# Kernel optimization log

Hardware: AMD Instinct MI355X
Metric: run time of the kernel (lower is better)

The kernel has to match this reference:

```python
import jax, jax.numpy as jnp
import numpy as np

POOL = (2, 2, 2)   # LPPool3d kernel == stride
KH, KW = 3, 3      # unfold kernel
EPS = 1e-6


def setup_inputs() -> dict:
    key = jax.random.key(0)
    k1, k2, k3 = jax.random.split(key, 3)
    x = jax.random.normal(k1, (32, 8, 4, 256, 256), dtype=jnp.float32)
    patch_dim = 8 * (4 // POOL[0]) * KH * KW  # 144
    out_dim = 128
    lin_w = jax.random.normal(k2, (out_dim, patch_dim), dtype=jnp.float32) * (1.0 / np.sqrt(patch_dim))
    lin_b = jax.random.normal(k3, (out_dim,), dtype=jnp.float32) * 0.01
    return {"x": x, "lin_w": lin_w, "lin_b": lin_b}


def reference(x, lin_w, lin_b):
    N, C, D, H, W = x.shape
    kd, kh, kw = POOL
    # LPPool3d with p=2, stride==kernel: (sum of squares in window)^(1/2)
    xr = (x * x).reshape(N, C, D // kd, kd, H // kh, kh, W // kw, kw)
    pooled = jnp.sqrt(xr.sum(axis=(3, 5, 7)))  # (N, C, Dp, Hp, Wp)
    Dp, Hp, Wp = pooled.shape[2], pooled.shape[3], pooled.shape[4]
    # merge depth into channels: permute(0,2,1,3,4).view(N, Dp*C, Hp, Wp)
    merged = pooled.transpose(0, 2, 1, 3, 4).reshape(N, Dp * C, Hp, Wp)
    MC = Dp * C
    Ho, Wo = Hp - KH + 1, Wp - KW + 1
    # im2col matching torch.nn.Unfold ordering: (channel, kh, kw) flattened
    slices = [merged[:, :, i:i + Ho, j:j + Wo] for i in range(KH) for j in range(KW)]
    patches = jnp.stack(slices, axis=2)                 # (N, MC, KH*KW, Ho, Wo)
    patches = patches.reshape(N, MC * KH * KW, Ho * Wo) # (N, patch_dim, L)
    patches = patches.transpose(0, 2, 1)                # (N, L, patch_dim)
    # per-patch linear + CELU (alpha=1)
    proj = jnp.einsum('nlk,ok->nlo', patches, lin_w) + lin_b  # (N, L, out_dim)
    act = jax.nn.celu(proj)
    # aggregate over patches, then L2-normalize with clamped norm
    agg = act.mean(axis=1)                              # (N, out_dim)
    norm = jnp.maximum(jnp.linalg.norm(agg, axis=1, keepdims=True), EPS)
    return agg / norm
```

## Files before the change

kernel.cpp:

```cpp
#include <hip/hip_runtime.h>
#include <math.h>

#define NB   32
#define C    8
#define D    4
#define H    256
#define W    256
#define HP   128
#define WP   128
#define MC   16
#define HO   126
#define WO   126
#define PATCH 144
#define OUTD 128
#define NL   (HO*WO)
#define HOG  6
#define NGRP (HO/HOG)
#define PROWS 9
#define BROW 168
#define NPOOLB 2048

typedef float  f32x4  __attribute__((ext_vector_type(4)));
typedef __bf16 bf16x8 __attribute__((ext_vector_type(8)));

__global__ __launch_bounds__(256, 4)
void pool_kernel(const float* __restrict__ x, __bf16* __restrict__ Pg) {
    int t = threadIdx.x;
    int wp2 = t & 63;
    int dph = (t >> 6) & 1;
    int g = blockIdx.x*2 + (t >> 7);
    int hp = g & 127, n = g >> 7;

    const float* xn = x + (size_t)n * (C*D*H*W) + (size_t)(2*dph) * (H*W)
                        + (2*hp)*W + 4*wp2;
    bf16x8 pk0, pk1;
#pragma unroll 2
    for (int c = 0; c < 8; c++) {
        const float* xb = xn + (size_t)c * (D*H*W);
        f32x4 a0 = *(const f32x4*)(xb);
        f32x4 a1 = *(const f32x4*)(xb + W);
        f32x4 a2 = *(const f32x4*)(xb + H*W);
        f32x4 a3 = *(const f32x4*)(xb + H*W + W);
        float s0 = a0.x*a0.x + a0.y*a0.y + a1.x*a1.x + a1.y*a1.y
                 + a2.x*a2.x + a2.y*a2.y + a3.x*a3.x + a3.y*a3.y;
        float s1 = a0.z*a0.z + a0.w*a0.w + a1.z*a1.z + a1.w*a1.w
                 + a2.z*a2.z + a2.w*a2.w + a3.z*a3.z + a3.w*a3.w;
        pk0[c] = (__bf16)sqrtf(s0);
        pk1[c] = (__bf16)sqrtf(s1);
    }
    __bf16* pr = Pg + ((size_t)n*HP + hp) * (WP*MC);
    *(bf16x8*)&pr[(2*wp2    )*16 + dph*8] = pk0;
    *(bf16x8*)&pr[(2*wp2 + 1)*16 + dph*8] = pk1;
}

__global__ __launch_bounds__(256, 2)
void gemm_kernel(const __bf16* __restrict__ Pg, const float* __restrict__ lin_w,
                 const float* __restrict__ lin_b, float* __restrict__ accg) {
    __shared__ __align__(16) char smem[PROWS*128*32 + OUTD*BROW*2];
    __bf16* Pl   = (__bf16*)smem;
    __bf16* Blds = (__bf16*)(smem + PROWS*128*32);

    int blk = blockIdx.x;
    int g = blk % NGRP, n = blk / NGRP;
    int ho0 = g * HOG;
    int t = threadIdx.x;
    int wave = t >> 6, lane = t & 63, quad = lane >> 4, l16 = lane & 15;

    {
        const f32x4* src = (const f32x4*)(Pg + ((size_t)n*HP + ho0) * (WP*MC));
        f32x4* dst = (f32x4*)Pl;
#pragma unroll
        for (int r = 0; r < 8; r++) dst[r*256 + t] = src[r*256 + t];
        f32x4 z = {};
        dst[8*256 + t] = z;
    }
    {
        int o = t & 127, kh = t >> 7;
#pragma unroll 4
        for (int kk = 0; kk < 80; kk++) {
            int kn = kh*80 + kk;
            int tap = kn >> 4, mc = kn & 15;
            float v = (tap < 9) ? lin_w[o*PATCH + mc*9 + tap] : 0.f;
            Blds[o*BROW + kn] = (__bf16)v;
        }
    }

    float lb[8];
#pragma unroll
    for (int nt = 0; nt < 8; nt++) lb[nt] = lin_b[nt*16 + l16];

    __syncthreads();

    float srun[8] = {0,0,0,0,0,0,0,0};
    int h8 = (quad & 1) * 8;
    int m0 = wave * 32 + l16;

    for (int hh = 0; hh < HOG; hh++) {
        f32x4 acc[2][8] = {};
#pragma unroll
        for (int ks = 0; ks < 5; ks++) {
            int tap = 2*ks + (quad >> 1);
            int it = (tap * 11) >> 5;
            int jt = tap - it * 3;
            bf16x8 afr[2];
#pragma unroll
            for (int mt = 0; mt < 2; mt++) {
                int m = m0 + mt*16;
                afr[mt] = *(const bf16x8*)&Pl[((hh + it)*128 + m + jt)*16 + h8];
            }
#pragma unroll
            for (int nt = 0; nt < 8; nt++) {
                bf16x8 bfr = *(const bf16x8*)&Blds[(nt*16 + l16)*BROW + ks*32 + quad*8];
                acc[0][nt] = __builtin_amdgcn_mfma_f32_16x16x32_bf16(afr[0], bfr, acc[0][nt], 0, 0, 0);
                acc[1][nt] = __builtin_amdgcn_mfma_f32_16x16x32_bf16(afr[1], bfr, acc[1][nt], 0, 0, 0);
            }
        }
#pragma unroll
        for (int nt = 0; nt < 8; nt++) {
            float s = 0.f;
#pragma unroll
            for (int mt = 0; mt < 2; mt++) {
                int mb = wave*32 + mt*16 + quad*4;
#pragma unroll
                for (int r = 0; r < 4; r++) {
                    float p = acc[mt][nt][r] + lb[nt];
                    float a = (p > 0.f) ? p : (__expf(p) - 1.f);
                    if (mb + r < WO) s += a;
                }
            }
            s += __shfl_xor(s, 16, 64);
            s += __shfl_xor(s, 32, 64);
            srun[nt] += s;
        }
    }

    __syncthreads();
    float* red = (float*)smem;
    if (quad == 0) {
#pragma unroll
        for (int nt = 0; nt < 8; nt++) red[wave*OUTD + nt*16 + l16] = srun[nt];
    }
    __syncthreads();
    if (t < OUTD) {
        float tot = red[t] + red[OUTD+t] + red[2*OUTD+t] + red[3*OUTD+t];
        atomicAdd(&accg[n*OUTD + t], tot);
    }
}

__global__ __launch_bounds__(256, 2)
void fused_kernel(const float* __restrict__ x, const float* __restrict__ lin_w,
                  const float* __restrict__ lin_b, float* __restrict__ accg) {
    __shared__ __align__(16) char smem[PROWS*128*32 + OUTD*BROW*2];
    __bf16* Pl   = (__bf16*)smem;
    __bf16* Blds = (__bf16*)(smem + PROWS*128*32);

    int blk = blockIdx.x;
    int g = blk % NGRP, n = blk / NGRP;
    int ho0 = g * HOG;
    int t = threadIdx.x;
    int wave = t >> 6, lane = t & 63, quad = lane >> 4, l16 = lane & 15;

    {
        int wp = t & 127, dph = t >> 7;
        const float* xn = x + (size_t)n * (C*D*H*W);
#pragma unroll 2
        for (int i = 0; i < 8; i++) {
            int hp = ho0 + i;
            bf16x8 pk;
#pragma unroll
            for (int c = 0; c < 8; c++) {
                const float* xb = xn + ((c*4 + 2*dph) * H + 2*hp) * W + 2*wp;
                float2 a0 = *(const float2*)(xb);
                float2 a1 = *(const float2*)(xb + W);
                float2 a2 = *(const float2*)(xb + H*W);
                float2 a3 = *(const float2*)(xb + H*W + W);
                float s = a0.x*a0.x + a0.y*a0.y + a1.x*a1.x + a1.y*a1.y
                        + a2.x*a2.x + a2.y*a2.y + a3.x*a3.x + a3.y*a3.y;
                pk[c] = (__bf16)sqrtf(s);
            }
            *(bf16x8*)&Pl[(i*128 + wp)*16 + dph*8] = pk;
        }
        bf16x8 z = {};
        *(bf16x8*)&Pl[(8*128 + wp)*16 + dph*8] = z;
    }
    {
        int o = t & 127, kh = t >> 7;
#pragma unroll 4
        for (int kk = 0; kk < 80; kk++) {
            int kn = kh*80 + kk;
            int tap = kn >> 4, mc = kn & 15;
            float v = (tap < 9) ? lin_w[o*PATCH + mc*9 + tap] : 0.f;
            Blds[o*BROW + kn] = (__bf16)v;
        }
    }

    float lb[8];
#pragma unroll
    for (int nt = 0; nt < 8; nt++) lb[nt] = lin_b[nt*16 + l16];

    __syncthreads();

    float srun[8] = {0,0,0,0,0,0,0,0};
    int h8 = (quad & 1) * 8;
    int m0 = wave * 32 + l16;

    for (int hh = 0; hh < HOG; hh++) {
        f32x4 acc[2][8] = {};
#pragma unroll
        for (int ks = 0; ks < 5; ks++) {
            int tap = 2*ks + (quad >> 1);
            int it = (tap * 11) >> 5;
            int jt = tap - it * 3;
            bf16x8 afr[2];
#pragma unroll
            for (int mt = 0; mt < 2; mt++) {
                int m = m0 + mt*16;
                afr[mt] = *(const bf16x8*)&Pl[((hh + it)*128 + m + jt)*16 + h8];
            }
#pragma unroll
            for (int nt = 0; nt < 8; nt++) {
                bf16x8 bfr = *(const bf16x8*)&Blds[(nt*16 + l16)*BROW + ks*32 + quad*8];
                acc[0][nt] = __builtin_amdgcn_mfma_f32_16x16x32_bf16(afr[0], bfr, acc[0][nt], 0, 0, 0);
                acc[1][nt] = __builtin_amdgcn_mfma_f32_16x16x32_bf16(afr[1], bfr, acc[1][nt], 0, 0, 0);
            }
        }
#pragma unroll
        for (int nt = 0; nt < 8; nt++) {
            float s = 0.f;
#pragma unroll
            for (int mt = 0; mt < 2; mt++) {
                int mb = wave*32 + mt*16 + quad*4;
#pragma unroll
                for (int r = 0; r < 4; r++) {
                    float p = acc[mt][nt][r] + lb[nt];
                    float a = (p > 0.f) ? p : (__expf(p) - 1.f);
                    if (mb + r < WO) s += a;
                }
            }
            s += __shfl_xor(s, 16, 64);
            s += __shfl_xor(s, 32, 64);
            srun[nt] += s;
        }
    }

    __syncthreads();
    float* red = (float*)smem;
    if (quad == 0) {
#pragma unroll
        for (int nt = 0; nt < 8; nt++) red[wave*OUTD + nt*16 + l16] = srun[nt];
    }
    __syncthreads();
    if (t < OUTD) {
        float tot = red[t] + red[OUTD+t] + red[2*OUTD+t] + red[3*OUTD+t];
        atomicAdd(&accg[n*OUTD + t], tot);
    }
}

__global__ void finalize_kernel(const float* __restrict__ acc, float* __restrict__ out) {
    int n = blockIdx.x;
    int o = threadIdx.x;
    float a = acc[n * OUTD + o] * (1.0f / (float)NL);
    float s = a * a;
#pragma unroll
    for (int off = 32; off > 0; off >>= 1) s += __shfl_down(s, off, 64);
    __shared__ float partial[2];
    if ((o & 63) == 0) partial[o >> 6] = s;
    __syncthreads();
    float norm = sqrtf(partial[0] + partial[1]);
    norm = fmaxf(norm, 1e-6f);
    out[n * OUTD + o] = a / norm;
}

extern "C" void kernel_launch(void* const* d_in, const int* in_sizes, int n_in,
                              void* d_out, int out_size, void* d_ws, size_t ws_size,
                              hipStream_t stream) {
    const float* x     = (const float*)d_in[0];
    const float* lin_w = (const float*)d_in[1];
    const float* lin_b = (const float*)d_in[2];
    float* out = (float*)d_out;

    float* acc = (float*)d_ws;
    hipMemsetAsync(acc, 0, NB * OUTD * sizeof(float), stream);

    const size_t PG_BYTES = (size_t)NB * HP * WP * MC * sizeof(__bf16);
    if (ws_size >= 16384 + PG_BYTES) {
        __bf16* Pg = (__bf16*)((char*)d_ws + 16384);
        pool_kernel<<<NPOOLB, 256, 0, stream>>>(x, Pg);
        gemm_kernel<<<NB * NGRP, 256, 0, stream>>>(Pg, lin_w, lin_b, acc);
    } else {
        fused_kernel<<<NB * NGRP, 256, 0, stream>>>(x, lin_w, lin_b, acc);
    }
    finalize_kernel<<<NB, OUTD, 0, stream>>>(acc, out);
}
```

Baseline: 429.1 us.

## Precompute bf16 weight tile once in pool kernel and reuse B fragments across two rows

```diff
diff --git a/kernel.cpp b/kernel.cpp
--- a/kernel.cpp
+++ b/kernel.cpp
@@ -24,11 +24,26 @@
 typedef __bf16 bf16x8 __attribute__((ext_vector_type(8)));
 
 __global__ __launch_bounds__(256, 4)
-void pool_kernel(const float* __restrict__ x, __bf16* __restrict__ Pg) {
+void pool_kernel(const float* __restrict__ x, const float* __restrict__ lin_w,
+                 __bf16* __restrict__ Pg, __bf16* __restrict__ Bw) {
     int t = threadIdx.x;
+    int b = blockIdx.x;
+
+    if (b == NPOOLB) {
+        int o = t & 127, kh = t >> 7;
+#pragma unroll 4
+        for (int kk = 0; kk < 80; kk++) {
+            int kn = kh*80 + kk;
+            int tap = kn >> 4, mc = kn & 15;
+            float v = (tap < 9) ? lin_w[o*PATCH + mc*9 + tap] : 0.f;
+            Bw[o*BROW + kn] = (__bf16)v;
+        }
+        return;
+    }
+
     int wp2 = t & 63;
     int dph = (t >> 6) & 1;
-    int g = blockIdx.x*2 + (t >> 7);
+    int g = b*2 + (t >> 7);
     int hp = g & 127, n = g >> 7;
 
     const float* xn = x + (size_t)n * (C*D*H*W) + (size_t)(2*dph) * (H*W)
@@ -54,7 +69,7 @@
 }
 
 __global__ __launch_bounds__(256, 2)
-void gemm_kernel(const __bf16* __restrict__ Pg, const float* __restrict__ lin_w,
+void gemm_kernel(const __bf16* __restrict__ Pg, const __bf16* __restrict__ Bw,
                  const float* __restrict__ lin_b, float* __restrict__ accg) {
     __shared__ __align__(16) char smem[PROWS*128*32 + OUTD*BROW*2];
     __bf16* Pl   = (__bf16*)smem;
@@ -73,16 +88,11 @@
         for (int r = 0; r < 8; r++) dst[r*256 + t] = src[r*256 + t];
         f32x4 z = {};
         dst[8*256 + t] = z;
-    }
-    {
-        int o = t & 127, kh = t >> 7;
-#pragma unroll 4
-        for (int kk = 0; kk < 80; kk++) {
-            int kn = kh*80 + kk;
-            int tap = kn >> 4, mc = kn & 15;
-            float v = (tap < 9) ? lin_w[o*PATCH + mc*9 + tap] : 0.f;
-            Blds[o*BROW + kn] = (__bf16)v;
-        }
+        const f32x4* bsrc = (const f32x4*)Bw;
+        f32x4* bdst = (f32x4*)Blds;
+#pragma unroll
+        for (int r = 0; r < 10; r++) bdst[r*256 + t] = bsrc[r*256 + t];
+        if (t < 128) bdst[10*256 + t] = bsrc[10*256 + t];
     }
 
     float lb[8];
@@ -95,42 +105,52 @@
     int h8 = (quad & 1) * 8;
     int m0 = wave * 32 + l16;
 
-    for (int hh = 0; hh < HOG; hh++) {
-        f32x4 acc[2][8] = {};
+    for (int hp = 0; hp < HOG/2; hp++) {
+        f32x4 acc[2][2][8] = {};
 #pragma unroll
         for (int ks = 0; ks < 5; ks++) {
             int tap = 2*ks + (quad >> 1);
             int it = (tap * 11) >> 5;
             int jt = tap - it * 3;
-            bf16x8 afr[2];
-#pragma unroll
-            for (int mt = 0; mt < 2; mt++) {
-                int m = m0 + mt*16;
-                afr[mt] = *(const bf16x8*)&Pl[((hh + it)*128 + m + jt)*16 + h8];
-            }
+            bf16x8 bfr[8];
+#pragma unroll
+            for (int nt = 0; nt < 8; nt++)
+                bfr[nt] = *(const bf16x8*)&Blds[(nt*16 + l16)*BROW + ks*32 + quad*8];
+            bf16x8 afr[2][2];
+#pragma unroll
+            for (int h = 0; h < 2; h++)
+#pragma unroll
+                for (int mt = 0; mt < 2; mt++) {
+                    int m = m0 + mt*16;
+                    afr[h][mt] = *(const bf16x8*)&Pl[((hp*2 + h + it)*128 + m + jt)*16 + h8];
+                }
 #pragma unroll
             for (int nt = 0; nt < 8; nt++) {
-                bf16x8 bfr = *(const bf16x8*)&Blds[(nt*16 + l16)*BROW + ks*32 + quad*8];
-                acc[0][nt] = __builtin_amdgcn_mfma_f32_16x16x32_bf16(afr[0], bfr, acc[0][nt], 0, 0, 0);
-                acc[1][nt] = __builtin_amdgcn_mfma_f32_16x16x32_bf16(afr[1], bfr, acc[1][nt], 0, 0, 0);
-            }
-        }
-#pragma unroll
-        for (int nt = 0; nt < 8; nt++) {
-            float s = 0.f;
-#pragma unroll
-            for (int mt = 0; mt < 2; mt++) {
-                int mb = wave*32 + mt*16 + quad*4;
-#pragma unroll
-                for (int r = 0; r < 4; r++) {
-                    float p = acc[mt][nt][r] + lb[nt];
-                    float a = (p > 0.f) ? p : (__expf(p) - 1.f);
-                    if (mb + r < WO) s += a;
+                acc[0][0][nt] = __builtin_amdgcn_mfma_f32_16x16x32_bf16(afr[0][0], bfr[nt], acc[0][0][nt], 0, 0, 0);
+                acc[0][1][nt] = __builtin_amdgcn_mfma_f32_16x16x32_bf16(afr[0][1], bfr[nt], acc[0][1][nt], 0, 0, 0);
+                acc[1][0][nt] = __builtin_amdgcn_mfma_f32_16x16x32_bf16(afr[1][0], bfr[nt], acc[1][0][nt], 0, 0, 0);
+                acc[1][1][nt] = __builtin_amdgcn_mfma_f32_16x16x32_bf16(afr[1][1], bfr[nt], acc[1][1][nt], 0, 0, 0);
+            }
+        }
+#pragma unroll
+        for (int h = 0; h < 2; h++) {
+#pragma unroll
+            for (int nt = 0; nt < 8; nt++) {
+                float s = 0.f;
+#pragma unroll
+                for (int mt = 0; mt < 2; mt++) {
+                    int mb = wave*32 + mt*16 + quad*4;
+#pragma unroll
+                    for (int r = 0; r < 4; r++) {
+                        float p = acc[h][mt][nt][r] + lb[nt];
+                        float a = (p > 0.f) ? p : (__expf(p) - 1.f);
+                        if (mb + r < WO) s += a;
+                    }
                 }
-            }
-            s += __shfl_xor(s, 16, 64);
-            s += __shfl_xor(s, 32, 64);
-            srun[nt] += s;
+                s += __shfl_xor(s, 16, 64);
+                s += __shfl_xor(s, 32, 64);
+                srun[nt] += s;
+            }
         }
     }
 
@@ -282,11 +302,13 @@
     float* acc = (float*)d_ws;
     hipMemsetAsync(acc, 0, NB * OUTD * sizeof(float), stream);
 
+    const size_t BW_BYTES = (size_t)OUTD * BROW * sizeof(__bf16);
     const size_t PG_BYTES = (size_t)NB * HP * WP * MC * sizeof(__bf16);
-    if (ws_size >= 16384 + PG_BYTES) {
-        __bf16* Pg = (__bf16*)((char*)d_ws + 16384);
-        pool_kernel<<<NPOOLB, 256, 0, stream>>>(x, Pg);
-        gemm_kernel<<<NB * NGRP, 256, 0, stream>>>(Pg, lin_w, lin_b, acc);
+    if (ws_size >= 16384 + BW_BYTES + PG_BYTES) {
+        __bf16* Bw = (__bf16*)((char*)d_ws + 16384);
+        __bf16* Pg = (__bf16*)((char*)d_ws + 16384 + BW_BYTES);
+        pool_kernel<<<NPOOLB + 1, 256, 0, stream>>>(x, lin_w, Pg, Bw);
+        gemm_kernel<<<NB * NGRP, 256, 0, stream>>>(Pg, Bw, lin_b, acc);
     } else {
         fused_kernel<<<NB * NGRP, 256, 0, stream>>>(x, lin_w, lin_b, acc);
     }
```

New measurement: 462.3 us. +7.7%, slower.
